# Kernel tuning notes

Hardware: AMD Instinct MI355X
Metric: run time of the kernel (lower is better)

The kernel has to match this reference:

```python
import jax, jax.numpy as jnp
import numpy as np
import math

B, N, D, O, H = 2, 3072, 64, 64, 4

def setup_inputs() -> dict:
    key = jax.random.key(0)
    ks = jax.random.split(key, 8)
    x = jax.random.normal(ks[0], (B, N, D), dtype=jnp.float32)
    edge_index = jax.random.randint(ks[1], (B, N, N), 0, 2, dtype=jnp.int32)
    s = 1.0 / math.sqrt(D)
    Wv = jax.random.uniform(ks[2], (H, D, O), jnp.float32, -s, s)
    bv = jax.random.uniform(ks[3], (H, O), jnp.float32, -s, s)
    Wq = jax.random.uniform(ks[4], (H, D, O), jnp.float32, -s, s)
    bq = jax.random.uniform(ks[5], (H, O), jnp.float32, -s, s)
    Wk = jax.random.uniform(ks[6], (H, D, O), jnp.float32, -s, s)
    bk = jax.random.uniform(ks[7], (H, O), jnp.float32, -s, s)
    return {"x": x, "edge_index": edge_index, "Wv": Wv, "bv": bv,
            "Wq": Wq, "bq": bq, "Wk": Wk, "bk": bk}

def reference(x, edge_index, Wv, bv, Wq, bq, Wk, bk):
    # x: [B,N,D]; edge_index: dense {0,1} adjacency [B,N,N]
    dk = jnp.asarray(math.sqrt(x.shape[-1]), x.dtype)
    v = jnp.einsum('bnd,hdo->bhno', x, Wv) + bv[None, :, None, :]
    q = jnp.einsum('bnd,hdo->bhno', x, Wq) + bq[None, :, None, :]
    k = jnp.einsum('bnd,hdo->bhno', x, Wk) + bk[None, :, None, :]
    scores = jnp.einsum('bhno,bhmo->bhnm', q, k) / dk        # [B,H,N,N]
    scores = jax.nn.leaky_relu(scores, 0.2)
    mask = (-1e10) * (1.0 - edge_index.astype(scores.dtype))  # [B,N,N]
    scores = scores + mask[:, None, :, :]
    prop = jax.nn.softmax(scores, axis=-1)
    # dropout on v omitted (inference mode: identity)
    feats = jnp.einsum('bhnm,bhmo->bhno', prop, v)            # [B,H,N,O]
    out = jnp.mean(feats, axis=1)                             # [B,N,O]
    return jax.nn.leaky_relu(out, 0.2)
```

## Files before the change

### kernel.cpp

```cpp
#include <hip/hip_runtime.h>
#include <hip/hip_bf16.h>
#include <cstdint>

#define Bc 2
#define Nc 3072
#define Hc 4
#define NW32 96
#define TILEB 8192
#define KSC 4
#define TPS (NW32/KSC)

typedef __bf16    bf16x8 __attribute__((ext_vector_type(8)));
typedef _Float16  f16x8  __attribute__((ext_vector_type(8)));
typedef float     f32x16 __attribute__((ext_vector_type(16)));

#define QSCALE 0.18033688f

static __device__ __forceinline__ f32x16 mfma32bf(bf16x8 a, bf16x8 b, f32x16 c) {
    return __builtin_amdgcn_mfma_f32_32x32x16_bf16(a, b, c, 0, 0, 0);
}
static __device__ __forceinline__ f32x16 mfma32h(f16x8 a, f16x8 b, f32x16 c) {
    return __builtin_amdgcn_mfma_f32_32x32x16_f16(a, b, c, 0, 0, 0);
}
static __device__ __forceinline__ void gload_lds16(const void* g, void* l) {
    __builtin_amdgcn_global_load_lds((const __attribute__((address_space(1))) void*)g,
                                     (__attribute__((address_space(3))) void*)l, 16, 0, 0);
}
static __device__ __forceinline__ uint32_t pkrtz(float lo, float hi) {
    uint32_t w;
    asm("v_cvt_pkrtz_f16_f32 %0, %1, %2" : "=v"(w) : "v"(lo), "v"(hi));
    return w;
}

static __device__ __forceinline__ void softmax_pack(const f32x16& sc, uint32_t mwh,
                                                    uint32_t W8[8], float& lsum)
{
    #pragma unroll
    for (int i = 0; i < 8; ++i) {
        const int bp0 = (2*i & 3) + 8*(2*i >> 2);
        float s0 = sc[2*i], s1 = sc[2*i + 1];
        float a0 = fmaxf(s0, 0.2f*s0);
        float a1 = fmaxf(s1, 0.2f*s1);
        float e0, e1;
        asm("v_exp_f32 %0, %1" : "=v"(e0) : "v"(a0));
        asm("v_exp_f32 %0, %1" : "=v"(e1) : "v"(a1));
        uint32_t m0 = (uint32_t)(((int)(mwh << (31 - bp0))) >> 31);
        uint32_t m1 = (uint32_t)(((int)(mwh << (30 - bp0))) >> 31);
        float p0 = __uint_as_float(__float_as_uint(e0) & m0);
        float p1 = __uint_as_float(__float_as_uint(e1) & m1);
        lsum += p0 + p1;
        W8[i] = pkrtz(p0, p1);
    }
}

static __device__ __forceinline__ void assemble_pa(uint32_t W8[8], f16x8& pa0, f16x8& pa1)
{
    uint32_t a0 = W8[0], a2 = W8[2], a1 = W8[1], a3 = W8[3];
    uint32_t b0 = W8[4], b2 = W8[6], b1 = W8[5], b3 = W8[7];
    asm("v_permlane32_swap_b32 %0, %1" : "+v"(a0), "+v"(a2));
    asm("v_permlane32_swap_b32 %0, %1" : "+v"(a1), "+v"(a3));
    asm("v_permlane32_swap_b32 %0, %1" : "+v"(b0), "+v"(b2));
    asm("v_permlane32_swap_b32 %0, %1" : "+v"(b1), "+v"(b3));
    union { uint32_t u[4]; f16x8 v; } u0, u1;
    u0.u[0] = a0; u0.u[1] = a1; u0.u[2] = a2; u0.u[3] = a3;
    u1.u[0] = b0; u1.u[1] = b1; u1.u[2] = b2; u1.u[3] = b3;
    pa0 = u0.v; pa1 = u1.v;
}

__global__ void prep_kernel(const float* __restrict__ Wq, const float* __restrict__ Wk,
                            const float* __restrict__ Wv,
                            const float* __restrict__ bq, const float* __restrict__ bk,
                            const float* __restrict__ bv,
                            __bf16* __restrict__ Wbh, __bf16* __restrict__ Wbl,
                            float* __restrict__ Bs)
{
    int i = blockIdx.x*256 + threadIdx.x;
    int d = i & 63, o = (i >> 6) & 63, h = (i >> 12) & 3, p = i >> 14;
    const float* W = (p == 0) ? Wq : (p == 1) ? Wk : Wv;
    float scale = (p == 0) ? QSCALE : 1.0f;
    float val = W[(h*64 + d)*64 + o] * scale;
    int idx = (((p*Hc + h)*64 + o) << 6) + d;
    __bf16 hi = (__bf16)val;
    Wbh[idx] = hi;
    Wbl[idx] = (__bf16)(val - (float)hi);
    if (i < 3*Hc*64) {
        int pp = i / (Hc*64), rest = i % (Hc*64);
        const float* B = (pp == 0) ? bq : (pp == 1) ? bk : bv;
        Bs[i] = B[rest] * ((pp == 0) ? QSCALE : 1.0f);
    }
}

__global__ __launch_bounds__(256) void qkv_mfma(
    const float* __restrict__ x,
    const __bf16* __restrict__ Wbh, const __bf16* __restrict__ Wbl,
    const float* __restrict__ Bs,
    _Float16* __restrict__ Qf, _Float16* __restrict__ Kf,
    _Float16* __restrict__ KVimg)
{
    const int lane = threadIdx.x & 63, w = threadIdx.x >> 6;
    const int l31 = lane & 31, hi = lane >> 5;
    int t = blockIdx.x;
    int nt = t % 48; t /= 48;
    int b  = t & 1;  t >>= 1;
    int p  = t % 3;
    int h  = t / 3;
    const int r0 = (w >> 1)*32, c0 = (w & 1)*32, n0 = nt*64;

    bf16x8 xh[4], xl[4], wh[4], wl[4];
    #pragma unroll
    for (int kk = 0; kk < 4; ++kk) {
        size_t xoff = (((size_t)(b*Nc + n0 + r0 + l31)) << 6) + kk*16 + hi*8;
        float4 f0 = *(const float4*)(x + xoff);
        float4 f1 = *(const float4*)(x + xoff + 4);
        float xs[8] = {f0.x, f0.y, f0.z, f0.w, f1.x, f1.y, f1.z, f1.w};
        #pragma unroll
        for (int j = 0; j < 8; ++j) {
            __bf16 hh = (__bf16)xs[j];
            xh[kk][j] = hh;
            xl[kk][j] = (__bf16)(xs[j] - (float)hh);
        }
        size_t woff = (((size_t)((p*Hc + h)*64 + c0 + l31)) << 6) + kk*16 + hi*8;
        wh[kk] = *(const bf16x8*)(Wbh + woff);
        wl[kk] = *(const bf16x8*)(Wbl + woff);
    }
    float bias = Bs[(p*Hc + h)*64 + c0 + l31];
    f32x16 acc;
    #pragma unroll
    for (int i = 0; i < 16; ++i) acc[i] = bias;
    #pragma unroll
    for (int kk = 0; kk < 4; ++kk) {
        acc = mfma32bf(xh[kk], wh[kk], acc);
        acc = mfma32bf(xl[kk], wh[kk], acc);
        acc = mfma32bf(xh[kk], wl[kk], acc);
    }
    const int bh = b*Hc + h;
    if (p < 2) {
        _Float16* dst = (p == 0) ? Qf : Kf;
        #pragma unroll
        for (int r = 0; r < 16; ++r) {
            int row = (r & 3) + 8*(r >> 2) + 4*hi;
            size_t idx = (((size_t)bh*Nc + n0 + r0 + row) << 6) + c0 + l31;
            dst[idx] = (_Float16)acc[r];
        }
    } else {
        const int t_img = (n0 + r0) >> 5;
        char* img = (char*)KVimg + (size_t)(bh*96 + t_img)*TILEB;
        #pragma unroll
        for (int grp = 0; grp < 2; ++grp) {
            uint32_t wH[4];
            #pragma unroll
            for (int j = 0; j < 4; ++j)
                wH[j] = pkrtz(acc[grp*8 + 2*j], acc[grp*8 + 2*j + 1]);
            asm("v_permlane32_swap_b32 %0, %1" : "+v"(wH[0]), "+v"(wH[2]));
            asm("v_permlane32_swap_b32 %0, %1" : "+v"(wH[1]), "+v"(wH[3]));
            const int kb = grp*2 + hi;
            const int o  = c0 + l31;
            uint4 gh = {wH[0], wH[1], wH[2], wH[3]};
            *(uint4*)(img + 4096 + ((kb*64 + o) << 4)) = gh;
        }
    }
}

__global__ void imgk_kernel(const _Float16* __restrict__ Kf, _Float16* __restrict__ KVimg)
{
    const int t = blockIdx.x % 96, bh = blockIdx.x / 96;
    char* img = (char*)KVimg + (size_t)(bh*96 + t)*TILEB;
    int dc = threadIdx.x & 7, key = threadIdx.x >> 3;
    size_t src = (((size_t)bh*Nc + t*32 + key) << 6) + dc*8;
    *(uint4*)(img + (dc*32 + key)*16) = *(const uint4*)(Kf + src);
}

__global__ void pack_kernel(const int* __restrict__ edge, uint32_t* __restrict__ pmT)
{
    int gw = blockIdx.x*4 + (threadIdx.x >> 6);
    int lane = threadIdx.x & 63;
    int ng = gw % 48; gw /= 48;
    int w  = gw % NW32; gw /= NW32;
    int b  = gw;
    int n = ng*64 + lane;
    const uint4* ep = (const uint4*)(edge + ((size_t)b*Nc + n)*Nc + w*32);
    uint32_t word = 0;
    #pragma unroll
    for (int i = 0; i < 8; ++i) {
        uint4 e = ep[i];
        word |= (e.x ? 1u : 0u) << (4*i);
        word |= (e.y ? 1u : 0u) << (4*i + 1);
        word |= (e.z ? 1u : 0u) << (4*i + 2);
        word |= (e.w ? 1u : 0u) << (4*i + 3);
    }
    pmT[((size_t)b*NW32 + w)*Nc + n] = word;
}

__global__ __launch_bounds__(512, 4) void attn_mfma(
    const _Float16* __restrict__ Qf,
    const _Float16* __restrict__ KVimg, const uint32_t* __restrict__ pmT,
    float* __restrict__ PA, float* __restrict__ PL)
{
    __shared__ __align__(16) char lds[3][2*TILEB];
    const int lane = threadIdx.x & 63, w = threadIdx.x >> 6;
    const int l31 = lane & 31, hi = lane >> 5;
    const int p2 = w >> 1;
    const int u  = w & 1;
    int gb = blockIdx.x;
    const int bh = gb & 7; gb >>= 3;
    const int qt = gb % 24;
    const int ks = gb / 24;
    const int b = bh >> 2;
    const int qrow0 = qt*128 + p2*32;
    const int t0 = ks*TPS;

    const uint32_t* pmp = pmT + ((size_t)b*NW32 + t0 + u)*Nc + qrow0 + l31;
    uint32_t mw_cur = pmp[0];
    __builtin_amdgcn_sched_barrier(0);
    const char* gbase = (const char*)KVimg + (size_t)(bh*96 + t0)*TILEB
                      + w*2048 + lane*16;
    #pragma unroll
    for (int g = 0; g < 2; ++g)
        gload_lds16(gbase + g*1024, &lds[0][w*2048 + g*1024]);

    f16x8 qf[4];
    #pragma unroll
    for (int kk = 0; kk < 4; ++kk) {
        size_t qoff = (((size_t)bh*Nc + qrow0 + l31) << 6) + kk*16 + hi*8;
        qf[kk] = *(const f16x8*)(Qf + qoff);
    }
    f32x16 fzero;
    #pragma unroll
    for (int i = 0; i < 16; ++i) fzero[i] = 0.f;

    f32x16 acc0 = fzero, acc1 = fzero;
    float lsum = 0.f;

    #pragma unroll 1
    for (int s = 0; s < 4; ++s) {
        #pragma unroll
        for (int j = 0; j < 3; ++j) {
            uint32_t mw_next = pmp[(size_t)(j + 1)*2*Nc];
            __builtin_amdgcn_sched_barrier(0);
            {
                char* ldst = &lds[(j + 1) % 3][w*2048];
                const char* gs = gbase + (size_t)(j + 1)*2*TILEB;
                #pragma unroll
                for (int g = 0; g < 2; ++g)
                    gload_lds16(gs + g*1024, ldst + g*1024);
            }
            asm volatile("s_waitcnt vmcnt(3)" ::: "memory");
            __builtin_amdgcn_s_barrier();
            asm volatile("" ::: "memory");
            const char* Lb = &lds[j][u*TILEB];

            f32x16 sc;
            __builtin_amdgcn_s_setprio(1);
            {
                f16x8 k0 = *(const f16x8*)(Lb + (hi << 9) + (l31 << 4));
                sc = mfma32h(k0, qf[0], fzero);
            }
            #pragma unroll
            for (int kk = 1; kk < 4; ++kk) {
                f16x8 k0 = *(const f16x8*)(Lb + ((kk*2 + hi) << 9) + (l31 << 4));
                sc = mfma32h(k0, qf[kk], sc);
            }
            __builtin_amdgcn_s_setprio(0);

            uint32_t W8[8];
            softmax_pack(sc, mw_cur >> (hi*4), W8, lsum);
            mw_cur = mw_next;
            f16x8 pa0, pa1;
            assemble_pa(W8, pa0, pa1);

            __builtin_amdgcn_s_setprio(1);
            #pragma unroll
            for (int kkp = 0; kkp < 2; ++kkp) {
                f16x8 pa = kkp ? pa1 : pa0;
                #pragma unroll
                for (int ot = 0; ot < 2; ++ot) {
                    f16x8 vh = *(const f16x8*)(Lb + 4096 + ((kkp*2 + hi) << 10)
                                               + ((ot*32 + l31) << 4));
                    if (ot == 0) acc0 = mfma32h(pa, vh, acc0);
                    else         acc1 = mfma32h(pa, vh, acc1);
                }
            }
            __builtin_amdgcn_s_setprio(0);
            asm volatile("" ::: "memory");
        }
        pmp   += (size_t)6*Nc;
        gbase += (size_t)6*TILEB;
    }

    asm volatile("s_waitcnt vmcnt(0)" ::: "memory");
    __syncthreads();

    float* xb  = (float*)&lds[0][0];
    float* xl2 = (float*)&lds[0][32*256*4];
    lsum += __shfl_xor(lsum, 32);
    if (u) {
        #pragma unroll
        for (int r = 0; r < 16; ++r) {
            xb[(r)      *256 + p2*64 + lane] = acc0[r];
            xb[(16 + r) *256 + p2*64 + lane] = acc1[r];
        }
        if (lane < 32) xl2[p2*32 + l31] = lsum;
    }
    __syncthreads();
    if (!u) {
        #pragma unroll
        for (int r = 0; r < 16; ++r) {
            acc0[r] += xb[(r)      *256 + p2*64 + lane];
            acc1[r] += xb[(16 + r) *256 + p2*64 + lane];
        }
        float* po = PA + (((size_t)(bh*KSC + ks)*Nc + qrow0) << 6);
        #pragma unroll
        for (int r = 0; r < 16; ++r) {
            int row = (r & 3) + 8*(r >> 2) + 4*hi;
            po[((size_t)row << 6) + l31]      = acc0[r];
            po[((size_t)row << 6) + 32 + l31] = acc1[r];
        }
        if (lane < 32) {
            float lt = lsum + xl2[p2*32 + l31];
            PL[(size_t)(bh*KSC + ks)*Nc + qrow0 + l31] = lt;
        }
    }
}

__global__ void merge_kernel(const float* __restrict__ PA, const float* __restrict__ PL,
                             float* __restrict__ out)
{
    int gid = blockIdx.x*256 + threadIdx.x;
    int o  = gid & 63;
    int bn = gid >> 6;
    int n  = bn % Nc;
    int b  = bn / Nc;
    float ft = 0.f;
    for (int h = 0; h < Hc; ++h) {
        int bh = b*Hc + h;
        float A = 0.f, L = 0.f;
        for (int ks = 0; ks < KSC; ++ks) {
            A += PA[(((size_t)(bh*KSC + ks)*Nc + n) << 6) + o];
            L += PL[(size_t)(bh*KSC + ks)*Nc + n];
        }
        ft += A / L;
    }
    ft *= 0.25f;
    out[((size_t)bn << 6) + o] = fmaxf(ft, 0.f) + 0.2f*fminf(ft, 0.f);
}

extern "C" void kernel_launch(void* const* d_in, const int* in_sizes, int n_in,
                              void* d_out, int out_size, void* d_ws, size_t ws_size,
                              hipStream_t stream)
{
    const float* x    = (const float*)d_in[0];
    const int*   edge = (const int*)d_in[1];
    const float* Wv   = (const float*)d_in[2];
    const float* bv   = (const float*)d_in[3];
    const float* Wq   = (const float*)d_in[4];
    const float* bq   = (const float*)d_in[5];
    const float* Wk   = (const float*)d_in[6];
    const float* bk   = (const float*)d_in[7];
    float* out = (float*)d_out;

    const size_t PROJ = (size_t)Bc*Hc*Nc*64;
    char* p = (char*)d_ws;
    __bf16* Wbh = (__bf16*)p;     p += 49152*2;
    __bf16* Wbl = (__bf16*)p;     p += 49152*2;
    float*  Bs  = (float*)p;      p += 4096;
    _Float16* Qf = (_Float16*)p;  p += PROJ*2;
    _Float16* Kf = (_Float16*)p;  p += PROJ*2;
    _Float16* KVimg = (_Float16*)p; p += (size_t)Bc*Hc*96*TILEB;
    uint32_t* pmT = (uint32_t*)p; p += (size_t)Bc*NW32*Nc*4;
    float* PA = (float*)p;        p += (size_t)Bc*Hc*KSC*Nc*64*4;
    float* PL = (float*)p;

    hipLaunchKernelGGL(prep_kernel, dim3(192),  dim3(256), 0, stream,
                       Wq, Wk, Wv, bq, bk, bv, Wbh, Wbl, Bs);
    hipLaunchKernelGGL(qkv_mfma,    dim3(1152), dim3(256), 0, stream,
                       x, Wbh, Wbl, Bs, Qf, Kf, KVimg);
    hipLaunchKernelGGL(imgk_kernel, dim3(Bc*Hc*96), dim3(256), 0, stream, Kf, KVimg);
    hipLaunchKernelGGL(pack_kernel, dim3(Bc*NW32*48/4), dim3(256), 0, stream, edge, pmT);
    hipLaunchKernelGGL(attn_mfma,   dim3(8*KSC*24), dim3(512), 0, stream,
                       Qf, KVimg, pmT, PA, PL);
    hipLaunchKernelGGL(merge_kernel, dim3((Bc*Nc*64)/256), dim3(256), 0, stream,
                       PA, PL, out);
}
```

Measured before the change: 78.44 us.

## Software-pipeline QK^T of next tile with softmax/PV of previous tile

Restructures the attention main loop so each step computes the score MFMAs for the current KV tile while doing softmax and PV for the previous tile, using a 4-deep LDS ring instead of 3. The loop is unrolled into a prologue, two 4-step iterations and an epilogue. The aim is to overlap the MFMA chains with the dependent softmax ALU work. In exchange it raises LDS use per block (4×16KB) and register pressure from holding an extra score accumulator, which may reduce occupancy under the 512×4 launch bounds.

Result: slower. 80.10 us (+2.1%).

```diff
diff --git a/kernel.cpp b/kernel.cpp
--- a/kernel.cpp
+++ b/kernel.cpp
@@ -191,12 +191,71 @@
     pmT[((size_t)b*NW32 + w)*Nc + n] = word;
 }
 
+template<int J, bool DOPREV>
+static __device__ __forceinline__ void attn_step(
+    char (&lds)[4][2*TILEB], const char* gbase, const uint32_t* pmp, int tnext,
+    int w, int u, int hi, int l31,
+    const f16x8 (&qf)[4], const f32x16& fzero,
+    f32x16& scP, uint32_t& mwA, uint32_t& mwB,
+    f32x16& acc0, f32x16& acc1, float& lsum)
+{
+    uint32_t mw_next = pmp[(size_t)tnext*2*Nc];
+    __builtin_amdgcn_sched_barrier(0);
+    {
+        char* ldst = &lds[(J + 1) & 3][w*2048];
+        const char* gs = gbase + (size_t)tnext*2*TILEB;
+        gload_lds16(gs, ldst);
+        gload_lds16(gs + 1024, ldst + 1024);
+    }
+    asm volatile("s_waitcnt vmcnt(3)" ::: "memory");
+    __builtin_amdgcn_s_barrier();
+    asm volatile("" ::: "memory");
+
+    const char* Lb = &lds[J][u*TILEB];
+    f32x16 scN;
+    __builtin_amdgcn_s_setprio(1);
+    {
+        f16x8 k0 = *(const f16x8*)(Lb + (hi << 9) + (l31 << 4));
+        scN = mfma32h(k0, qf[0], fzero);
+    }
+    #pragma unroll
+    for (int kk = 1; kk < 4; ++kk) {
+        f16x8 k0 = *(const f16x8*)(Lb + ((kk*2 + hi) << 9) + (l31 << 4));
+        scN = mfma32h(k0, qf[kk], scN);
+    }
+    __builtin_amdgcn_s_setprio(0);
+
+    if (DOPREV) {
+        uint32_t W8[8];
+        softmax_pack(scP, mwA >> (hi*4), W8, lsum);
+        f16x8 pa0, pa1;
+        assemble_pa(W8, pa0, pa1);
+        const char* Lp = &lds[(J + 3) & 3][u*TILEB];
+        __builtin_amdgcn_s_setprio(1);
+        #pragma unroll
+        for (int kkp = 0; kkp < 2; ++kkp) {
+            f16x8 pa = kkp ? pa1 : pa0;
+            #pragma unroll
+            for (int ot = 0; ot < 2; ++ot) {
+                f16x8 vh = *(const f16x8*)(Lp + 4096 + ((kkp*2 + hi) << 10)
+                                           + ((ot*32 + l31) << 4));
+                if (ot == 0) acc0 = mfma32h(pa, vh, acc0);
+                else         acc1 = mfma32h(pa, vh, acc1);
+            }
+        }
+        __builtin_amdgcn_s_setprio(0);
+    }
+    scP = scN;
+    mwA = mwB; mwB = mw_next;
+    asm volatile("" ::: "memory");
+}
+
 __global__ __launch_bounds__(512, 4) void attn_mfma(
     const _Float16* __restrict__ Qf,
     const _Float16* __restrict__ KVimg, const uint32_t* __restrict__ pmT,
     float* __restrict__ PA, float* __restrict__ PL)
 {
-    __shared__ __align__(16) char lds[3][2*TILEB];
+    __shared__ __align__(16) char lds[4][2*TILEB];
     const int lane = threadIdx.x & 63, w = threadIdx.x >> 6;
     const int l31 = lane & 31, hi = lane >> 5;
     const int p2 = w >> 1;
@@ -210,13 +269,13 @@
     const int t0 = ks*TPS;
 
     const uint32_t* pmp = pmT + ((size_t)b*NW32 + t0 + u)*Nc + qrow0 + l31;
-    uint32_t mw_cur = pmp[0];
+    uint32_t mwA = 0;
+    uint32_t mwB = pmp[0];
     __builtin_amdgcn_sched_barrier(0);
     const char* gbase = (const char*)KVimg + (size_t)(bh*96 + t0)*TILEB
                       + w*2048 + lane*16;
-    #pragma unroll
-    for (int g = 0; g < 2; ++g)
-        gload_lds16(gbase + g*1024, &lds[0][w*2048 + g*1024]);
+    gload_lds16(gbase, &lds[0][w*2048]);
+    gload_lds16(gbase + 1024, &lds[0][w*2048 + 1024]);
 
     f16x8 qf[4];
     #pragma unroll
@@ -228,70 +287,58 @@
     #pragma unroll
     for (int i = 0; i < 16; ++i) fzero[i] = 0.f;
 
-    f32x16 acc0 = fzero, acc1 = fzero;
+    f32x16 acc0 = fzero, acc1 = fzero, scP = fzero;
     float lsum = 0.f;
 
+    attn_step<0, false>(lds, gbase, pmp, 1, w, u, hi, l31, qf, fzero,
+                        scP, mwA, mwB, acc0, acc1, lsum);
+    attn_step<1, true >(lds, gbase, pmp, 2, w, u, hi, l31, qf, fzero,
+                        scP, mwA, mwB, acc0, acc1, lsum);
+    attn_step<2, true >(lds, gbase, pmp, 3, w, u, hi, l31, qf, fzero,
+                        scP, mwA, mwB, acc0, acc1, lsum);
+    attn_step<3, true >(lds, gbase, pmp, 4, w, u, hi, l31, qf, fzero,
+                        scP, mwA, mwB, acc0, acc1, lsum);
+    pmp   += (size_t)8*Nc;
+    gbase += (size_t)8*TILEB;
+
     #pragma unroll 1
-    for (int s = 0; s < 4; ++s) {
-        #pragma unroll
-        for (int j = 0; j < 3; ++j) {
-            uint32_t mw_next = pmp[(size_t)(j + 1)*2*Nc];
-            __builtin_amdgcn_sched_barrier(0);
-            {
-                char* ldst = &lds[(j + 1) % 3][w*2048];
-                const char* gs = gbase + (size_t)(j + 1)*2*TILEB;
-                #pragma unroll
-                for (int g = 0; g < 2; ++g)
-                    gload_lds16(gs + g*1024, ldst + g*1024);
+    for (int s = 0; s < 2; ++s) {
+        attn_step<0, true>(lds, gbase, pmp, 1, w, u, hi, l31, qf, fzero,
+                           scP, mwA, mwB, acc0, acc1, lsum);
+        attn_step<1, true>(lds, gbase, pmp, 2, w, u, hi, l31, qf, fzero,
+                           scP, mwA, mwB, acc0, acc1, lsum);
+        attn_step<2, true>(lds, gbase, pmp, 3, w, u, hi, l31, qf, fzero,
+                           scP, mwA, mwB, acc0, acc1, lsum);
+        attn_step<3, true>(lds, gbase, pmp, 4, w, u, hi, l31, qf, fzero,
+                           scP, mwA, mwB, acc0, acc1, lsum);
+        pmp   += (size_t)8*Nc;
+        gbase += (size_t)8*TILEB;
+    }
+
+    {
+        uint32_t W8[8];
+        softmax_pack(scP, mwA >> (hi*4), W8, lsum);
+        f16x8 pa0, pa1;
+        assemble_pa(W8, pa0, pa1);
+        const char* Lp = &lds[3][u*TILEB];
+        #pragma unroll
+        for (int kkp = 0; kkp < 2; ++kkp) {
+            f16x8 pa = kkp ? pa1 : pa0;
+            #pragma unroll
+            for (int ot = 0; ot < 2; ++ot) {
+                f16x8 vh = *(const f16x8*)(Lp + 4096 + ((kkp*2 + hi) << 10)
+                                           + ((ot*32 + l31) << 4));
+                if (ot == 0) acc0 = mfma32h(pa, vh, acc0);
+                else         acc1 = mfma32h(pa, vh, acc1);
             }
-            asm volatile("s_waitcnt vmcnt(3)" ::: "memory");
-            __builtin_amdgcn_s_barrier();
-            asm volatile("" ::: "memory");
-            const char* Lb = &lds[j][u*TILEB];
-
-            f32x16 sc;
-            __builtin_amdgcn_s_setprio(1);
-            {
-                f16x8 k0 = *(const f16x8*)(Lb + (hi << 9) + (l31 << 4));
-                sc = mfma32h(k0, qf[0], fzero);
-            }
-            #pragma unroll
-            for (int kk = 1; kk < 4; ++kk) {
-                f16x8 k0 = *(const f16x8*)(Lb + ((kk*2 + hi) << 9) + (l31 << 4));
-                sc = mfma32h(k0, qf[kk], sc);
-            }
-            __builtin_amdgcn_s_setprio(0);
-
-            uint32_t W8[8];
-            softmax_pack(sc, mw_cur >> (hi*4), W8, lsum);
-            mw_cur = mw_next;
-            f16x8 pa0, pa1;
-            assemble_pa(W8, pa0, pa1);
-
-            __builtin_amdgcn_s_setprio(1);
-            #pragma unroll
-            for (int kkp = 0; kkp < 2; ++kkp) {
-                f16x8 pa = kkp ? pa1 : pa0;
-                #pragma unroll
-                for (int ot = 0; ot < 2; ++ot) {
-                    f16x8 vh = *(const f16x8*)(Lb + 4096 + ((kkp*2 + hi) << 10)
-                                               + ((ot*32 + l31) << 4));
-                    if (ot == 0) acc0 = mfma32h(pa, vh, acc0);
-                    else         acc1 = mfma32h(pa, vh, acc1);
-                }
-            }
-            __builtin_amdgcn_s_setprio(0);
-            asm volatile("" ::: "memory");
-        }
-        pmp   += (size_t)6*Nc;
-        gbase += (size_t)6*TILEB;
+        }
     }
 
     asm volatile("s_waitcnt vmcnt(0)" ::: "memory");
     __syncthreads();
 
     float* xb  = (float*)&lds[0][0];
-    float* xl2 = (float*)&lds[0][32*256*4];
+    float* xl2 = (float*)&lds[2][0];
     lsum += __shfl_xor(lsum, 32);
     if (u) {
         #pragma unroll
```

## Replace LDS-staged KV pipeline with direct register double-buffered global loads

Applied to the files above, without the earlier changes.

The attention kernel stops staging K/V tiles through shared memory with async global-to-LDS loads and barriers. Each wave now loads its K/V fragments straight from global memory into registers, double-buffered A/B across tiles. The two-wave split of key tiles and its LDS reduction are removed, so each wave handles all key tiles for its 32 query rows and the block shrinks from 512 to 256 threads. This removes barriers and LDS traffic, but every wave fetches the same K/V data separately through L1/L2, raises register pressure, and does one redundant prefetch of tile 0 on the last iteration.

New measurement: 78.65 us. No clear change (+0.3%).

```diff
diff --git a/kernel.cpp b/kernel.cpp
--- a/kernel.cpp
+++ b/kernel.cpp
@@ -21,10 +21,6 @@
 }
 static __device__ __forceinline__ f32x16 mfma32h(f16x8 a, f16x8 b, f32x16 c) {
     return __builtin_amdgcn_mfma_f32_32x32x16_f16(a, b, c, 0, 0, 0);
-}
-static __device__ __forceinline__ void gload_lds16(const void* g, void* l) {
-    __builtin_amdgcn_global_load_lds((const __attribute__((address_space(1))) void*)g,
-                                     (__attribute__((address_space(3))) void*)l, 16, 0, 0);
 }
 static __device__ __forceinline__ uint32_t pkrtz(float lo, float hi) {
     uint32_t w;
@@ -65,6 +61,45 @@
     u0.u[0] = a0; u0.u[1] = a1; u0.u[2] = a2; u0.u[3] = a3;
     u1.u[0] = b0; u1.u[1] = b1; u1.u[2] = b2; u1.u[3] = b3;
     pa0 = u0.v; pa1 = u1.v;
+}
+
+static __device__ __forceinline__ void load_subtile(const char* gt, int hi, int l31,
+                                                    f16x8 (&K)[4], f16x8 (&V)[4])
+{
+    #pragma unroll
+    for (int kk = 0; kk < 4; ++kk)
+        K[kk] = *(const f16x8*)(gt + ((kk*2 + hi) << 9) + (l31 << 4));
+    #pragma unroll
+    for (int i = 0; i < 4; ++i) {
+        const int kkp = i >> 1, ot = i & 1;
+        V[i] = *(const f16x8*)(gt + 4096 + ((kkp*2 + hi) << 10) + ((ot*32 + l31) << 4));
+    }
+}
+
+static __device__ __forceinline__ void compute_subtile(
+    const f16x8 (&K)[4], const f16x8 (&V)[4], uint32_t mw, int hi,
+    const f16x8 (&qf)[4], const f32x16& fzero,
+    f32x16& acc0, f32x16& acc1, float& lsum)
+{
+    f32x16 sc;
+    __builtin_amdgcn_s_setprio(1);
+    sc = mfma32h(K[0], qf[0], fzero);
+    sc = mfma32h(K[1], qf[1], sc);
+    sc = mfma32h(K[2], qf[2], sc);
+    sc = mfma32h(K[3], qf[3], sc);
+    __builtin_amdgcn_s_setprio(0);
+
+    uint32_t W8[8];
+    softmax_pack(sc, mw >> (hi*4), W8, lsum);
+    f16x8 pa0, pa1;
+    assemble_pa(W8, pa0, pa1);
+
+    __builtin_amdgcn_s_setprio(1);
+    acc0 = mfma32h(pa0, V[0], acc0);
+    acc1 = mfma32h(pa0, V[1], acc1);
+    acc0 = mfma32h(pa1, V[2], acc0);
+    acc1 = mfma32h(pa1, V[3], acc1);
+    __builtin_amdgcn_s_setprio(0);
 }
 
 __global__ void prep_kernel(const float* __restrict__ Wq, const float* __restrict__ Wk,
@@ -191,32 +226,23 @@
     pmT[((size_t)b*NW32 + w)*Nc + n] = word;
 }
 
-__global__ __launch_bounds__(512, 4) void attn_mfma(
+__global__ __launch_bounds__(256, 3) void attn_mfma(
     const _Float16* __restrict__ Qf,
     const _Float16* __restrict__ KVimg, const uint32_t* __restrict__ pmT,
     float* __restrict__ PA, float* __restrict__ PL)
 {
-    __shared__ __align__(16) char lds[3][2*TILEB];
     const int lane = threadIdx.x & 63, w = threadIdx.x >> 6;
     const int l31 = lane & 31, hi = lane >> 5;
-    const int p2 = w >> 1;
-    const int u  = w & 1;
     int gb = blockIdx.x;
     const int bh = gb & 7; gb >>= 3;
     const int qt = gb % 24;
     const int ks = gb / 24;
     const int b = bh >> 2;
-    const int qrow0 = qt*128 + p2*32;
+    const int qrow0 = qt*128 + w*32;
     const int t0 = ks*TPS;
 
-    const uint32_t* pmp = pmT + ((size_t)b*NW32 + t0 + u)*Nc + qrow0 + l31;
-    uint32_t mw_cur = pmp[0];
-    __builtin_amdgcn_sched_barrier(0);
-    const char* gbase = (const char*)KVimg + (size_t)(bh*96 + t0)*TILEB
-                      + w*2048 + lane*16;
-    #pragma unroll
-    for (int g = 0; g < 2; ++g)
-        gload_lds16(gbase + g*1024, &lds[0][w*2048 + g*1024]);
+    const uint32_t* pmp = pmT + ((size_t)b*NW32 + t0)*Nc + qrow0 + l31;
+    const char* gt = (const char*)KVimg + (size_t)(bh*96 + t0)*TILEB;
 
     f16x8 qf[4];
     #pragma unroll
@@ -231,95 +257,32 @@
     f32x16 acc0 = fzero, acc1 = fzero;
     float lsum = 0.f;
 
+    f16x8 KA[4], VA[4], KB[4], VB[4];
+    uint32_t mwA, mwB;
+    load_subtile(gt, hi, l31, KA, VA);
+    mwA = pmp[0];
+
     #pragma unroll 1
-    for (int s = 0; s < 4; ++s) {
-        #pragma unroll
-        for (int j = 0; j < 3; ++j) {
-            uint32_t mw_next = pmp[(size_t)(j + 1)*2*Nc];
-            __builtin_amdgcn_sched_barrier(0);
-            {
-                char* ldst = &lds[(j + 1) % 3][w*2048];
-                const char* gs = gbase + (size_t)(j + 1)*2*TILEB;
-                #pragma unroll
-                for (int g = 0; g < 2; ++g)
-                    gload_lds16(gs + g*1024, ldst + g*1024);
-            }
-            asm volatile("s_waitcnt vmcnt(3)" ::: "memory");
-            __builtin_amdgcn_s_barrier();
-            asm volatile("" ::: "memory");
-            const char* Lb = &lds[j][u*TILEB];
-
-            f32x16 sc;
-            __builtin_amdgcn_s_setprio(1);
-            {
-                f16x8 k0 = *(const f16x8*)(Lb + (hi << 9) + (l31 << 4));
-                sc = mfma32h(k0, qf[0], fzero);
-            }
-            #pragma unroll
-            for (int kk = 1; kk < 4; ++kk) {
-                f16x8 k0 = *(const f16x8*)(Lb + ((kk*2 + hi) << 9) + (l31 << 4));
-                sc = mfma32h(k0, qf[kk], sc);
-            }
-            __builtin_amdgcn_s_setprio(0);
-
-            uint32_t W8[8];
-            softmax_pack(sc, mw_cur >> (hi*4), W8, lsum);
-            mw_cur = mw_next;
-            f16x8 pa0, pa1;
-            assemble_pa(W8, pa0, pa1);
-
-            __builtin_amdgcn_s_setprio(1);
-            #pragma unroll
-            for (int kkp = 0; kkp < 2; ++kkp) {
-                f16x8 pa = kkp ? pa1 : pa0;
-                #pragma unroll
-                for (int ot = 0; ot < 2; ++ot) {
-                    f16x8 vh = *(const f16x8*)(Lb + 4096 + ((kkp*2 + hi) << 10)
-                                               + ((ot*32 + l31) << 4));
-                    if (ot == 0) acc0 = mfma32h(pa, vh, acc0);
-                    else         acc1 = mfma32h(pa, vh, acc1);
-                }
-            }
-            __builtin_amdgcn_s_setprio(0);
-            asm volatile("" ::: "memory");
-        }
-        pmp   += (size_t)6*Nc;
-        gbase += (size_t)6*TILEB;
-    }
-
-    asm volatile("s_waitcnt vmcnt(0)" ::: "memory");
-    __syncthreads();
-
-    float* xb  = (float*)&lds[0][0];
-    float* xl2 = (float*)&lds[0][32*256*4];
+    for (int j = 0; j < TPS/2; ++j) {
+        load_subtile(gt + (size_t)(2*j + 1)*TILEB, hi, l31, KB, VB);
+        mwB = pmp[(size_t)(2*j + 1)*Nc];
+        compute_subtile(KA, VA, mwA, hi, qf, fzero, acc0, acc1, lsum);
+        const int tn = (2*j + 2 < TPS) ? (2*j + 2) : 0;
+        load_subtile(gt + (size_t)tn*TILEB, hi, l31, KA, VA);
+        mwA = pmp[(size_t)tn*Nc];
+        compute_subtile(KB, VB, mwB, hi, qf, fzero, acc0, acc1, lsum);
+    }
+
     lsum += __shfl_xor(lsum, 32);
-    if (u) {
-        #pragma unroll
-        for (int r = 0; r < 16; ++r) {
-            xb[(r)      *256 + p2*64 + lane] = acc0[r];
-            xb[(16 + r) *256 + p2*64 + lane] = acc1[r];
-        }
-        if (lane < 32) xl2[p2*32 + l31] = lsum;
-    }
-    __syncthreads();
-    if (!u) {
-        #pragma unroll
-        for (int r = 0; r < 16; ++r) {
-            acc0[r] += xb[(r)      *256 + p2*64 + lane];
-            acc1[r] += xb[(16 + r) *256 + p2*64 + lane];
-        }
-        float* po = PA + (((size_t)(bh*KSC + ks)*Nc + qrow0) << 6);
-        #pragma unroll
-        for (int r = 0; r < 16; ++r) {
-            int row = (r & 3) + 8*(r >> 2) + 4*hi;
-            po[((size_t)row << 6) + l31]      = acc0[r];
-            po[((size_t)row << 6) + 32 + l31] = acc1[r];
-        }
-        if (lane < 32) {
-            float lt = lsum + xl2[p2*32 + l31];
-            PL[(size_t)(bh*KSC + ks)*Nc + qrow0 + l31] = lt;
-        }
-    }
+    float* po = PA + (((size_t)(bh*KSC + ks)*Nc + qrow0) << 6);
+    #pragma unroll
+    for (int r = 0; r < 16; ++r) {
+        int row = (r & 3) + 8*(r >> 2) + 4*hi;
+        po[((size_t)row << 6) + l31]      = acc0[r];
+        po[((size_t)row << 6) + 32 + l31] = acc1[r];
+    }
+    if (lane < 32)
+        PL[(size_t)(bh*KSC + ks)*Nc + qrow0 + l31] = lsum;
 }
 
 __global__ void merge_kernel(const float* __restrict__ PA, const float* __restrict__ PL,
@@ -376,7 +339,7 @@
                        x, Wbh, Wbl, Bs, Qf, Kf, KVimg);
     hipLaunchKernelGGL(imgk_kernel, dim3(Bc*Hc*96), dim3(256), 0, stream, Kf, KVimg);
     hipLaunchKernelGGL(pack_kernel, dim3(Bc*NW32*48/4), dim3(256), 0, stream, edge, pmT);
-    hipLaunchKernelGGL(attn_mfma,   dim3(8*KSC*24), dim3(512), 0, stream,
+    hipLaunchKernelGGL(attn_mfma,   dim3(8*KSC*24), dim3(256), 0, stream,
                        Qf, KVimg, pmT, PA, PL);
     hipLaunchKernelGGL(merge_kernel, dim3((Bc*Nc*64)/256), dim3(256), 0, stream,
                        PA, PL, out);
```
